# Optimization experiments

Measured on AMD Instinct MI355X. Metric: run time of the kernel, lower is better.

The kernel has to match this reference:

```python
import jax, jax.numpy as jnp
import numpy as np

B, N, L, K = 2, 16384, 256, 4
DIN, DOUT, DLAT, H, A, NH = 2, 3, 64, 128, 32, 4
PI = float(np.pi)

def _lin(key, din, dout, std=None):
    k1, k2 = jax.random.split(key)
    if std is None:
        lim = 1.0 / np.sqrt(din)
        w = jax.random.uniform(k1, (din, dout), minval=-lim, maxval=lim)
        b = jax.random.uniform(k2, (dout,), minval=-lim, maxval=lim)
        return w, b
    return jax.random.normal(k1, (din, dout)) * std

def setup_inputs() -> dict:
    key = jax.random.key(0)
    ks = jax.random.split(key, 16)
    x = jax.random.uniform(ks[0], (B, N, DIN)) * 2.0 - 1.0
    p = jax.random.uniform(ks[1], (B, L, DIN)) * 2.0 - 1.0
    c = jax.random.normal(ks[2], (B, L, DLAT))
    g = jax.random.uniform(ks[3], (B, L, 1)) * 0.5 + 0.1
    W_stem, b_stem = _lin(ks[4], DLAT, H)
    Wq_sin = _lin(ks[5], DIN, H // 2, std=2.0)
    Wq1, bq1 = _lin(ks[6], H + DIN, H)
    Wq2, bq2 = _lin(ks[7], H, NH * A)
    Wv_sin = _lin(ks[8], DIN, H // 2, std=20.0)
    Wv1, bv1 = _lin(ks[9], H + DIN, H)
    Wv2, bv2 = _lin(ks[10], H, 2 * H)
    Wk, bk = _lin(ks[11], H, NH * A)
    Wv, bv = _lin(ks[12], H, NH * H)
    Wo1, bo1 = _lin(ks[13], NH * H, NH * H)
    Wo2, bo2 = _lin(ks[14], NH * H, DOUT)
    return dict(x=x, p=p, c=c, g=g, W_stem=W_stem, b_stem=b_stem,
                Wq_sin=Wq_sin, Wq1=Wq1, bq1=bq1, Wq2=Wq2, bq2=bq2,
                Wv_sin=Wv_sin, Wv1=Wv1, bv1=bv1, Wv2=Wv2, bv2=bv2,
                Wk=Wk, bk=bk, Wv=Wv, bv=bv, Wo1=Wo1, bo1=bo1, Wo2=Wo2, bo2=bo2)

def _sin_emb(coords, W):
    c = PI * (coords + 1.0)
    e = c @ W
    return jnp.sin(jnp.concatenate([c, e, e + PI / 2.0], axis=-1))

def _emb_mlp(coords, Wsin, W1, b1, W2, b2):
    h = _sin_emb(coords, Wsin)
    h = jax.nn.gelu(h @ W1 + b1, approximate=False)
    return h @ W2 + b2

def _gather(t, idx):
    # t: [B,L,D], idx: [B,N,K] -> [B,N,K,D]
    return jax.vmap(lambda tb, ib: tb[ib])(t, idx)

def reference(x, p, c, g, W_stem, b_stem, Wq_sin, Wq1, bq1, Wq2, bq2,
              Wv_sin, Wv1, bv1, Wv2, bv2, Wk, bk, Wv, bv, Wo1, bo1, Wo2, bo2):
    c = c @ W_stem + b_stem                       # [B,L,H]
    k = c @ Wk + bk                               # [B,L,NH*A]
    rel_pos = x[:, :, None, :] - p[:, None, :, :] # [B,N,L,2]
    zx = jnp.sum(rel_pos ** 2, axis=-1)           # [B,N,L]
    idx = jnp.argsort(zx, axis=-1)[:, :, :K]      # [B,N,K]
    zx_k = jnp.take_along_axis(zx, idx, axis=2)[..., None]            # [B,N,K,1]
    rel_k = jnp.take_along_axis(rel_pos, idx[..., None], axis=2)      # [B,N,K,2]
    c_k = _gather(c, idx)                         # [B,N,K,H]
    k_k = _gather(k, idx)                         # [B,N,K,NH*A]
    g_k = _gather(g, idx)                         # [B,N,K,1]
    q = _emb_mlp(rel_k, Wq_sin, Wq1, bq1, Wq2, bq2)                   # [B,N,K,NH*A]
    vgb = _emb_mlp(rel_k, Wv_sin, Wv1, bv1, Wv2, bv2)                 # [B,N,K,2H]
    v_g, v_b = vgb[..., :H], vgb[..., H:]
    v = (c_k * v_g + v_b) @ Wv + bv               # [B,N,K,NH*H]
    q = q.reshape(B, N, K, NH, A)
    k_k = k_k.reshape(B, N, K, NH, A)
    v = v.reshape(B, N, K, NH, H)
    logits = jnp.sum(q * k_k, axis=-1, keepdims=True) \
             - ((1.0 / g_k ** 2) * zx_k)[..., None, :]                # [B,N,K,NH,1]
    att = jax.nn.softmax(logits, axis=2)
    y = jnp.sum(att * v, axis=2).reshape(B, N, NH * H)
    y = jax.nn.gelu(y @ Wo1 + bo1, approximate=False)
    return y @ Wo2 + bo2                          # [B,N,3]
```

## Files before the change

kernel.cpp:

```cpp
#include <hip/hip_runtime.h>
#include <math.h>

typedef unsigned short U16;
typedef unsigned int u32;
typedef unsigned long long u64;
typedef __attribute__((ext_vector_type(8))) short short8;
typedef __attribute__((ext_vector_type(4))) float f4;

#define LPTS   256
#define MFMA16(a,b,c) __builtin_amdgcn_mfma_f32_16x16x32_bf16(a, b, c, 0, 0, 0)

__device__ __forceinline__ float bf2f(U16 u) {
  return __uint_as_float(((unsigned int)u) << 16);
}
__device__ __forceinline__ U16 f2bf(float f) {
  unsigned int x = __float_as_uint(f);
  return (U16)((x + 0x7fffu + ((x >> 16) & 1u)) >> 16);
}
__device__ __forceinline__ float gelu_f(float v) {
  float z = fabsf(v) * 0.70710678f;
  float t = __builtin_amdgcn_rcpf(fmaf(0.3275911f, z, 1.0f));
  float poly = t * fmaf(t, fmaf(t, fmaf(t, fmaf(t, 1.061405429f, -1.453152027f),
                                        1.421413741f), -0.284496736f), 0.254829592f);
  float e = __expf(-z * z);
  float erf_abs = fmaf(-poly, e, 1.0f);
  float erf_s = copysignf(erf_abs, v);
  return 0.5f * v * (1.0f + erf_s);
}
__device__ __forceinline__ void ins4(u32& k0, u32& k1, u32& k2, u32& k3, u32 key) {
  if (key < k3) {
    if (key < k0)      { k3 = k2; k2 = k1; k1 = k0; k0 = key; }
    else if (key < k1) { k3 = k2; k2 = k1; k1 = key; }
    else if (key < k2) { k3 = k2; k2 = key; }
    else               { k3 = key; }
  }
}
__device__ __forceinline__ float ldf(const void* s, int i, int mode) {
  return mode ? bf2f(((const U16*)s)[i]) : ((const float*)s)[i];
}
__device__ __forceinline__ int wave_sniff(const void* w4) {
  int lane = threadIdx.x & 63;
  float v = bf2f(((const U16*)w4)[2 * lane]);
  u64 m = __ballot(fabsf(v) <= 0.1251f);
  return (__popcll(m) >= 56) ? 1 : 0;
}

struct PackArgs {
  const void* src[6];
  int K[6], N[6], KS[6];
  int base[7];
};

__global__ __launch_bounds__(256) void enf_prep(PackArgs pa,
    const void* c, const void* Wst, const void* bst, const void* Wkp, const void* bkp,
    float* __restrict__ cp_ws, float* __restrict__ kk_ws, U16* __restrict__ P)
{
  __shared__ float c_s[2][64];
  __shared__ float cp_s[2][128];
  const int t = threadIdx.x;
  const int mode = wave_sniff(Wst);
  const int bid = blockIdx.x;
  if (bid < 204) {
    int u = bid * 256 + t;
    if (u < pa.base[6]) {
      int s = 0;
      while (u >= pa.base[s + 1]) ++s;
      int rel = u - pa.base[s];
      int lane8 = rel & 63, rest = rel >> 6;
      int ks = rest % pa.KS[s], nt = rest / pa.KS[s];
      int kb = ks * 32 + ((lane8 >> 4) * 8);
      int n  = nt * 16 + (lane8 & 15);
      U16 vv[8];
#pragma unroll
      for (int j = 0; j < 8; ++j) {
        int k = kb + j;
        U16 v = 0;
        if (k < pa.K[s]) {
          int off = k * pa.N[s] + n;
          v = mode ? ((const U16*)pa.src[s])[off] : f2bf(((const float*)pa.src[s])[off]);
        }
        vv[j] = v;
      }
      *(short8*)(P + (size_t)u * 8) = *(short8*)vv;
    }
  } else {
    const int half = t >> 7, tl = t & 127;
    const int row = (bid - 204) * 2 + half;
    if (tl < 64) c_s[half][tl] = ldf(c, row * 64 + tl, mode);
    __syncthreads();
    float acc = 0.f;
#pragma unroll 8
    for (int i = 0; i < 64; ++i) acc = fmaf(c_s[half][i], ldf(Wst, i * 128 + tl, mode), acc);
    float cpv = acc + ldf(bst, tl, mode);
    cp_s[half][tl] = cpv;
    cp_ws[row * 128 + tl] = cpv;
    __syncthreads();
    acc = 0.f;
#pragma unroll 8
    for (int i = 0; i < 128; ++i) acc = fmaf(cp_s[half][i], ldf(Wkp, i * 128 + tl, mode), acc);
    kk_ws[row * 128 + tl] = acc + ldf(bkp, tl, mode);
  }
}

__global__ __launch_bounds__(512, 8) void enf_main(
    const void* __restrict__ w4,
    const void* __restrict__ x, const void* __restrict__ p, const void* __restrict__ g,
    const void* __restrict__ Wq_sin, const void* __restrict__ Wv_sin,
    const U16* __restrict__ PWq1, const void* __restrict__ bq1,
    const U16* __restrict__ PWq2, const void* __restrict__ bq2,
    const U16* __restrict__ PWv1, const void* __restrict__ bv1,
    const U16* __restrict__ PWv2, const void* __restrict__ bv2,
    const U16* __restrict__ PWv, const void* __restrict__ bv,
    const U16* __restrict__ PWo1, const void* __restrict__ bo1,
    const void* __restrict__ Wo2, const void* __restrict__ bo2,
    const float* __restrict__ cp_ws, const float* __restrict__ kk_ws,
    void* __restrict__ outp)
{
  __shared__ __align__(16) U16 poolS[64 * 168];
  __shared__ __align__(16) U16 poolH[64 * 132];
  __shared__ float wsin_s[128];
  __shared__ float xq[32];
  __shared__ float selDx[64], selDy[64], selB[64];
  __shared__ float att_s[64 * 4];
  __shared__ U16   selL[64];

  const int t = threadIdx.x;
  const int w = t >> 6, lane = t & 63;
  const int quad = lane >> 4, cl = lane & 15;
  const int qbase = blockIdx.x * 16;
  const int b = qbase >> 14;
  const int mode = wave_sniff(w4);
  float* p_sh = (float*)poolS;

  if (t < 32) xq[t] = ldf(x, qbase * 2 + t, mode);
  if (t < 128) wsin_s[t] = ldf(Wq_sin, t, mode);
  p_sh[t] = ldf(p, b * LPTS * 2 + t, mode);
  __syncthreads();

  {
    const int q = t >> 5;
    const float x0 = xq[q * 2 + 0], x1 = xq[q * 2 + 1];
    const int j = t & 31;
    u32 k0 = ~0u, k1 = ~0u, k2 = ~0u, k3 = ~0u;
#pragma unroll
    for (int s = 0; s < 8; ++s) {
      const int l = j * 8 + s;
      float dx = __fsub_rn(x0, p_sh[l * 2 + 0]);
      float dy = __fsub_rn(x1, p_sh[l * 2 + 1]);
      float d  = __fadd_rn(__fmul_rn(dx, dx), __fmul_rn(dy, dy));
      u32 key = (__float_as_uint(d) & 0xFFFFFF00u) | (u32)l;
      ins4(k0, k1, k2, k3, key);
    }
#pragma unroll
    for (int d = 1; d <= 16; d <<= 1) {
      u32 p0 = __shfl_xor(k0, d, 32);
      u32 p1 = __shfl_xor(k1, d, 32);
      u32 p2 = __shfl_xor(k2, d, 32);
      u32 p3 = __shfl_xor(k3, d, 32);
      ins4(k0, k1, k2, k3, p0); ins4(k0, k1, k2, k3, p1);
      ins4(k0, k1, k2, k3, p2); ins4(k0, k1, k2, k3, p3);
    }
    if (j == 0) {
      u32 sel[4] = { k0, k1, k2, k3 };
#pragma unroll
      for (int k = 0; k < 4; ++k) {
        int l = (int)(sel[k] & 255u);
        int r = q * 4 + k;
        selL[r]  = (U16)l;
        float dx = __fsub_rn(x0, p_sh[l * 2 + 0]);
        float dy = __fsub_rn(x1, p_sh[l * 2 + 1]);
        float zx = __fadd_rn(__fmul_rn(dx, dx), __fmul_rn(dy, dy));
        selDx[r] = dx;
        selDy[r] = dy;
        float gf = ldf(g, b * LPTS + l, mode);
        selB[r]  = __fmul_rn(1.0f / __fmul_rn(gf, gf), zx);
      }
    }
  }
  __syncthreads();

  {
    const int r = t >> 3, ln = t & 7;
    const float dx = selDx[r], dy = selDy[r];
    const float c0 = 3.14159274f * (dx + 1.0f);
    const float c1 = 3.14159274f * (dy + 1.0f);
    if (ln == 0) poolS[r * 168 + 0] = f2bf(__sinf(c0));
    if (ln == 1) poolS[r * 168 + 1] = f2bf(__sinf(c1));
#pragma unroll 1
    for (int i = ln; i < 64; i += 8) {
      float e = __fadd_rn(__fmul_rn(c0, wsin_s[i]), __fmul_rn(c1, wsin_s[64 + i]));
      poolS[r * 168 + 2 + i]  = f2bf(__sinf(e));
      poolS[r * 168 + 66 + i] = f2bf(__sinf(e + 1.57079637f));
    }
#pragma unroll 1
    for (int i = 130 + ln; i < 160; i += 8) poolS[r * 168 + i] = 0;
  }
  __syncthreads();

  if (t < 128) wsin_s[t] = ldf(Wv_sin, t, mode);
  {
    f4 acc[4] = {{0,0,0,0},{0,0,0,0},{0,0,0,0},{0,0,0,0}};
    const U16* pb0 = PWq1 + ((w * 5) * 64 + lane) * 8;
    short8 b0 = *(const short8*)(pb0);
#pragma unroll 1
    for (int ks = 0; ks < 5; ++ks) {
      short8 n0 = *(const short8*)(pb0 + (ks + 1) * 512);
#pragma unroll
      for (int mt = 0; mt < 4; ++mt) {
        short8 a = *(const short8*)(poolS + (mt * 16 + cl) * 168 + quad * 8 + ks * 32);
        acc[mt] = MFMA16(a, b0, acc[mt]);
      }
      b0 = n0;
    }
    int col = w * 16 + cl;
    float bb = ldf(bq1, col, mode);
#pragma unroll
    for (int mt = 0; mt < 4; ++mt)
#pragma unroll
      for (int reg = 0; reg < 4; ++reg)
        poolH[(mt * 16 + quad * 4 + reg) * 132 + col] = f2bf(gelu_f(acc[mt][reg] + bb));
  }
  __syncthreads();

  if (w < 4) {
    const int wl = w;
    f4 acc[2][4] = {{{0,0,0,0},{0,0,0,0},{0,0,0,0},{0,0,0,0}},
                    {{0,0,0,0},{0,0,0,0},{0,0,0,0},{0,0,0,0}}};
    const U16* pb0 = PWq2 + ((2 * wl + 0) * 4 * 64 + lane) * 8;
    const U16* pb1 = PWq2 + ((2 * wl + 1) * 4 * 64 + lane) * 8;
    short8 b0 = *(const short8*)(pb0);
    short8 b1 = *(const short8*)(pb1);
#pragma unroll 1
    for (int ks = 0; ks < 4; ++ks) {
      short8 n0 = *(const short8*)(pb0 + (ks + 1) * 512);
      short8 n1 = *(const short8*)(pb1 + (ks + 1) * 512);
#pragma unroll
      for (int mt = 0; mt < 4; ++mt) {
        short8 a = *(const short8*)(poolH + (mt * 16 + cl) * 132 + quad * 8 + ks * 32);
        acc[0][mt] = MFMA16(a, b0, acc[0][mt]);
        acc[1][mt] = MFMA16(a, b1, acc[1][mt]);
      }
      b0 = n0; b1 = n1;
    }
    const float bq2c0 = ldf(bq2, (2 * wl + 0) * 16 + cl, mode);
    const float bq2c1 = ldf(bq2, (2 * wl + 1) * 16 + cl, mode);
    const float* kkb = kk_ws + (size_t)b * LPTS * 128;
#pragma unroll
    for (int mt = 0; mt < 4; ++mt) {
      float part[4];
#pragma unroll
      for (int reg = 0; reg < 4; ++reg) {
        int r = mt * 16 + quad * 4 + reg;
        const float* kr = kkb + selL[r] * 128;
        float q0 = acc[0][mt][reg] + bq2c0;
        float q1 = acc[1][mt][reg] + bq2c1;
        part[reg] = __fmul_rn(q0, kr[(2 * wl + 0) * 16 + cl]);
        part[reg] = fmaf(q1, kr[(2 * wl + 1) * 16 + cl], part[reg]);
      }
#pragma unroll
      for (int d = 1; d <= 8; d <<= 1) {
        part[0] += __shfl_xor(part[0], d, 16);
        part[1] += __shfl_xor(part[1], d, 16);
        part[2] += __shfl_xor(part[2], d, 16);
        part[3] += __shfl_xor(part[3], d, 16);
      }
      if (cl == 0) {
        int q = mt * 4 + quad;
        float lg[4];
#pragma unroll
        for (int reg = 0; reg < 4; ++reg)
          lg[reg] = part[reg] - selB[q * 4 + reg];
        float m = fmaxf(fmaxf(lg[0], lg[1]), fmaxf(lg[2], lg[3]));
        float e0 = __expf(lg[0] - m), e1 = __expf(lg[1] - m);
        float e2 = __expf(lg[2] - m), e3 = __expf(lg[3] - m);
        float s = ((e0 + e1) + e2) + e3;
        att_s[(q * 4 + 0) * 4 + wl] = e0 / s;
        att_s[(q * 4 + 1) * 4 + wl] = e1 / s;
        att_s[(q * 4 + 2) * 4 + wl] = e2 / s;
        att_s[(q * 4 + 3) * 4 + wl] = e3 / s;
      }
    }
  } else {
    const int tt = t - 256;
    const int r = tt >> 2, ln = tt & 3;
    const float dx = selDx[r], dy = selDy[r];
    const float c0 = 3.14159274f * (dx + 1.0f);
    const float c1 = 3.14159274f * (dy + 1.0f);
    if (ln == 0) poolS[r * 168 + 0] = f2bf(__sinf(c0));
    if (ln == 1) poolS[r * 168 + 1] = f2bf(__sinf(c1));
#pragma unroll 1
    for (int i = ln; i < 64; i += 4) {
      float e = __fadd_rn(__fmul_rn(c0, wsin_s[i]), __fmul_rn(c1, wsin_s[64 + i]));
      poolS[r * 168 + 2 + i]  = f2bf(__sinf(e));
      poolS[r * 168 + 66 + i] = f2bf(__sinf(e + 1.57079637f));
    }
#pragma unroll 1
    for (int i = 130 + ln; i < 160; i += 4) poolS[r * 168 + i] = 0;
  }
  __syncthreads();

  {
    f4 acc[4] = {{0,0,0,0},{0,0,0,0},{0,0,0,0},{0,0,0,0}};
    const U16* pb0 = PWv1 + ((w * 5) * 64 + lane) * 8;
    short8 b0 = *(const short8*)(pb0);
#pragma unroll 1
    for (int ks = 0; ks < 5; ++ks) {
      short8 n0 = *(const short8*)(pb0 + (ks + 1) * 512);
#pragma unroll
      for (int mt = 0; mt < 4; ++mt) {
        short8 a = *(const short8*)(poolS + (mt * 16 + cl) * 168 + quad * 8 + ks * 32);
        acc[mt] = MFMA16(a, b0, acc[mt]);
      }
      b0 = n0;
    }
    int col = w * 16 + cl;
    float bb = ldf(bv1, col, mode);
#pragma unroll
    for (int mt = 0; mt < 4; ++mt)
#pragma unroll
      for (int reg = 0; reg < 4; ++reg)
        poolH[(mt * 16 + quad * 4 + reg) * 132 + col] = f2bf(gelu_f(acc[mt][reg] + bb));
  }
  __syncthreads();

  {
    f4 ag[4] = {{0,0,0,0},{0,0,0,0},{0,0,0,0},{0,0,0,0}};
    f4 ab[4] = {{0,0,0,0},{0,0,0,0},{0,0,0,0},{0,0,0,0}};
    const U16* pg = PWv2 + ((w * 4) * 64 + lane) * 8;
    const U16* pb = PWv2 + (((8 + w) * 4) * 64 + lane) * 8;
    short8 bg = *(const short8*)(pg);
    short8 bb2 = *(const short8*)(pb);
#pragma unroll 1
    for (int ks = 0; ks < 4; ++ks) {
      short8 ng = *(const short8*)(pg + (ks + 1) * 512);
      short8 nb = *(const short8*)(pb + (ks + 1) * 512);
#pragma unroll
      for (int mt = 0; mt < 4; ++mt) {
        short8 a = *(const short8*)(poolH + (mt * 16 + cl) * 132 + quad * 8 + ks * 32);
        ag[mt] = MFMA16(a, bg, ag[mt]);
        ab[mt] = MFMA16(a, bb2, ab[mt]);
      }
      bg = ng; bb2 = nb;
    }
    int col = w * 16 + cl;
    float bgb = ldf(bv2, col, mode), bbb = ldf(bv2, 128 + col, mode);
#pragma unroll
    for (int mt = 0; mt < 4; ++mt)
#pragma unroll
      for (int reg = 0; reg < 4; ++reg) {
        int row = mt * 16 + quad * 4 + reg;
        float cp = cp_ws[(b * LPTS + selL[row]) * 128 + col];
        float vin = __fadd_rn(__fmul_rn(cp, ag[mt][reg] + bgb), ab[mt][reg] + bbb);
        poolS[row * 132 + col] = f2bf(vin);
      }
  }
  __syncthreads();

  {
    const int gqh = t >> 3, sl = t & 7;
    const int q = gqh & 15, h = gqh >> 4;
    float a0 = att_s[(q * 4 + 0) * 4 + h];
    float a1 = att_s[(q * 4 + 1) * 4 + h];
    float a2 = att_s[(q * 4 + 2) * 4 + h];
    float a3 = att_s[(q * 4 + 3) * 4 + h];
#pragma unroll 1
    for (int j = 0; j < 4; ++j) {
      int e0 = j * 32 + sl * 4;
      ushort4 v0 = *(const ushort4*)(poolS + (q * 4 + 0) * 132 + e0);
      ushort4 v1 = *(const ushort4*)(poolS + (q * 4 + 1) * 132 + e0);
      ushort4 v2 = *(const ushort4*)(poolS + (q * 4 + 2) * 132 + e0);
      ushort4 v3 = *(const ushort4*)(poolS + (q * 4 + 3) * 132 + e0);
      ushort4 o;
      o.x = f2bf(fmaf(a3, bf2f(v3.x), fmaf(a2, bf2f(v2.x), fmaf(a1, bf2f(v1.x), a0 * bf2f(v0.x)))));
      o.y = f2bf(fmaf(a3, bf2f(v3.y), fmaf(a2, bf2f(v2.y), fmaf(a1, bf2f(v1.y), a0 * bf2f(v0.y)))));
      o.z = f2bf(fmaf(a3, bf2f(v3.z), fmaf(a2, bf2f(v2.z), fmaf(a1, bf2f(v1.z), a0 * bf2f(v0.z)))));
      o.w = f2bf(fmaf(a3, bf2f(v3.w), fmaf(a2, bf2f(v2.w), fmaf(a1, bf2f(v1.w), a0 * bf2f(v0.w)))));
      *(ushort4*)(poolH + (h * 16 + q) * 132 + e0) = o;
    }
  }
  __syncthreads();

  U16* ySt = poolS;
  {
    f4 acc5[4] = {{0,0,0,0},{0,0,0,0},{0,0,0,0},{0,0,0,0}};
    const int h = w >> 1;
    const int nt0 = h * 8 + (w & 1) * 4;
    const U16* a5p = poolH + (h * 16 + cl) * 132 + quad * 8;
    short8 cb[4], nb[4];
#pragma unroll
    for (int ntl = 0; ntl < 4; ++ntl)
      cb[ntl] = *(const short8*)(PWv + ((nt0 + ntl) * 4 * 64 + lane) * 8);
#pragma unroll 1
    for (int ks = 0; ks < 4; ++ks) {
#pragma unroll
      for (int ntl = 0; ntl < 4; ++ntl)
        nb[ntl] = *(const short8*)(PWv + (((nt0 + ntl) * 4 + ks + 1) * 64 + lane) * 8);
      short8 a = *(const short8*)(a5p + ks * 32);
#pragma unroll
      for (int ntl = 0; ntl < 4; ++ntl) acc5[ntl] = MFMA16(a, cb[ntl], acc5[ntl]);
#pragma unroll
      for (int ntl = 0; ntl < 4; ++ntl) cb[ntl] = nb[ntl];
    }
#pragma unroll
    for (int ntl = 0; ntl < 4; ++ntl) {
      int col = (nt0 + ntl) * 16 + cl;
      float bbv = ldf(bv, col, mode);
#pragma unroll
      for (int reg = 0; reg < 4; ++reg) {
        int q = quad * 4 + reg;
        ySt[q * 520 + col] = f2bf(acc5[ntl][reg] + bbv);
      }
    }
  }
  __syncthreads();

  {
    f4 acc[4] = {{0,0,0,0},{0,0,0,0},{0,0,0,0},{0,0,0,0}};
    const U16* aP = ySt + cl * 520 + quad * 8;
    const U16* bP = PWo1 + ((w * 4) * 16 * 64 + lane) * 8;
    short8 cb[4], nb[4];
#pragma unroll
    for (int ntl = 0; ntl < 4; ++ntl)
      cb[ntl] = *(const short8*)(bP + (ntl * 16) * 512);
#pragma unroll 1
    for (int ks = 0; ks < 16; ++ks) {
#pragma unroll
      for (int ntl = 0; ntl < 4; ++ntl)
        nb[ntl] = *(const short8*)(bP + (ntl * 16 + ks + 1) * 512);
      short8 a = *(const short8*)(aP + ks * 32);
#pragma unroll
      for (int ntl = 0; ntl < 4; ++ntl) acc[ntl] = MFMA16(a, cb[ntl], acc[ntl]);
#pragma unroll
      for (int ntl = 0; ntl < 4; ++ntl) cb[ntl] = nb[ntl];
    }
    float oacc[4][3];
#pragma unroll
    for (int reg = 0; reg < 4; ++reg) { oacc[reg][0]=0.f; oacc[reg][1]=0.f; oacc[reg][2]=0.f; }
#pragma unroll
    for (int ntl = 0; ntl < 4; ++ntl) {
      int col = (w * 4 + ntl) * 16 + cl;
      float bb = ldf(bo1, col, mode);
      float w0 = ldf(Wo2, col * 3 + 0, mode);
      float w1 = ldf(Wo2, col * 3 + 1, mode);
      float w2 = ldf(Wo2, col * 3 + 2, mode);
#pragma unroll
      for (int reg = 0; reg < 4; ++reg) {
        float y2 = gelu_f(acc[ntl][reg] + bb);
        oacc[reg][0] = fmaf(y2, w0, oacc[reg][0]);
        oacc[reg][1] = fmaf(y2, w1, oacc[reg][1]);
        oacc[reg][2] = fmaf(y2, w2, oacc[reg][2]);
      }
    }
    float* obuf = (float*)poolH;
#pragma unroll
    for (int reg = 0; reg < 4; ++reg)
#pragma unroll
      for (int cix = 0; cix < 3; ++cix) {
        float v = oacc[reg][cix];
        v += __shfl_xor(v, 1);
        v += __shfl_xor(v, 2);
        v += __shfl_xor(v, 4);
        v += __shfl_xor(v, 8);
        if (cl == 0) obuf[(w * 16 + quad * 4 + reg) * 3 + cix] = v;
      }
  }
  __syncthreads();
  if (t < 48) {
    float* obuf = (float*)poolH;
    int row = t / 3, cix = t - row * 3;
    float s = obuf[row * 3 + cix];
#pragma unroll
    for (int ww = 1; ww < 8; ++ww) s += obuf[(ww * 16 + row) * 3 + cix];
    float ov = s + ldf(bo2, cix, mode);
    int pos = (qbase + row) * 3 + cix;
    if (mode) ((U16*)outp)[pos] = f2bf(ov);
    else      ((float*)outp)[pos] = ov;
  }
}

extern "C" void kernel_launch(void* const* d_in, const int* in_sizes, int n_in,
                              void* d_out, int out_size, void* d_ws, size_t ws_size,
                              hipStream_t stream) {
  (void)in_sizes; (void)n_in; (void)out_size; (void)ws_size;

  float* ws     = (float*)d_ws;
  float* cp_ws  = ws;
  float* kk_ws  = ws + 65536;
  U16*   Pbase  = (U16*)(ws + 131072);
  U16*   PWq1   = Pbase + 0;
  U16*   PWq2   = Pbase + 20480;
  U16*   PWv1   = Pbase + 36864;
  U16*   PWv2   = Pbase + 57344;
  U16*   PWv    = Pbase + 90112;
  U16*   PWo1   = Pbase + 155648;

  PackArgs pa;
  const int psrc[6] = {7, 9, 12, 14, 18, 20};
  static const int pK[6]  = {130, 128, 130, 128, 128, 512};
  static const int pN[6]  = {128, 128, 128, 256, 512, 512};
  static const int pKS[6] = {5, 4, 5, 4, 4, 16};
  static const int pB8[7] = {0, 2560, 4608, 7168, 11264, 19456, 52224};
  for (int i = 0; i < 6; ++i) {
    pa.src[i] = d_in[psrc[i]];
    pa.K[i] = pK[i]; pa.N[i] = pN[i]; pa.KS[i] = pKS[i]; pa.base[i] = pB8[i];
  }
  pa.base[6] = pB8[6];

  hipLaunchKernelGGL(enf_prep, dim3(460), dim3(256), 0, stream,
                     pa, d_in[2], d_in[4], d_in[5], d_in[16], d_in[17],
                     cp_ws, kk_ws, Pbase);
  hipLaunchKernelGGL(enf_main, dim3(2048), dim3(512), 0, stream,
                     d_in[4],
                     d_in[0], d_in[1], d_in[3],
                     d_in[6], d_in[11],
                     PWq1, d_in[8],  PWq2, d_in[10],
                     PWv1, d_in[13], PWv2, d_in[15],
                     PWv,  d_in[19],
                     PWo1, d_in[21], d_in[22], d_in[23],
                     cp_ws, kk_ws, (void*)d_out);
}
```

Before: 281.3 us.

## Process 32 queries per block to double MFMA reuse of weight fragments

Doubles the number of query points per workgroup from 16 to 32 (128 neighbor rows), halving the grid and giving each wave twice as many M-tiles per loaded weight fragment across all the MLP and projection GEMMs. The goal is to halve the global/L2 traffic for the packed weights per query and amortise per-block setup such as the p load and the kNN staging. In exchange, LDS use and accumulator registers roughly double, and launch bounds drop to 4 blocks per SM, which lowers occupancy and latency hiding.

```diff
diff --git a/kernel.cpp b/kernel.cpp
--- a/kernel.cpp
+++ b/kernel.cpp
@@ -102,7 +102,7 @@
   }
 }
 
-__global__ __launch_bounds__(512, 8) void enf_main(
+__global__ __launch_bounds__(512, 4) void enf_main(
     const void* __restrict__ w4,
     const void* __restrict__ x, const void* __restrict__ p, const void* __restrict__ g,
     const void* __restrict__ Wq_sin, const void* __restrict__ Wv_sin,
@@ -116,35 +116,34 @@
     const float* __restrict__ cp_ws, const float* __restrict__ kk_ws,
     void* __restrict__ outp)
 {
-  __shared__ __align__(16) U16 poolS[64 * 168];
-  __shared__ __align__(16) U16 poolH[64 * 132];
+  __shared__ __align__(16) U16 poolS[128 * 168];
+  __shared__ __align__(16) U16 poolH[128 * 132];
   __shared__ float wsin_s[128];
-  __shared__ float xq[32];
-  __shared__ float selDx[64], selDy[64], selB[64];
-  __shared__ float att_s[64 * 4];
-  __shared__ U16   selL[64];
-
+  __shared__ float xq[64];
+  __shared__ float selDx[128], selDy[128], selB[128];
+  __shared__ float att_s[128 * 4];
+  __shared__ U16   selL[128];
   const int t = threadIdx.x;
   const int w = t >> 6, lane = t & 63;
   const int quad = lane >> 4, cl = lane & 15;
-  const int qbase = blockIdx.x * 16;
+  const int qbase = blockIdx.x * 32;
   const int b = qbase >> 14;
   const int mode = wave_sniff(w4);
   float* p_sh = (float*)poolS;
 
-  if (t < 32) xq[t] = ldf(x, qbase * 2 + t, mode);
+  if (t < 64) xq[t] = ldf(x, qbase * 2 + t, mode);
   if (t < 128) wsin_s[t] = ldf(Wq_sin, t, mode);
   p_sh[t] = ldf(p, b * LPTS * 2 + t, mode);
   __syncthreads();
 
   {
-    const int q = t >> 5;
+    const int q = t >> 4;
     const float x0 = xq[q * 2 + 0], x1 = xq[q * 2 + 1];
-    const int j = t & 31;
+    const int j = t & 15;
     u32 k0 = ~0u, k1 = ~0u, k2 = ~0u, k3 = ~0u;
 #pragma unroll
-    for (int s = 0; s < 8; ++s) {
-      const int l = j * 8 + s;
+    for (int s = 0; s < 16; ++s) {
+      const int l = j * 16 + s;
       float dx = __fsub_rn(x0, p_sh[l * 2 + 0]);
       float dy = __fsub_rn(x1, p_sh[l * 2 + 1]);
       float d  = __fadd_rn(__fmul_rn(dx, dx), __fmul_rn(dy, dy));
@@ -152,11 +151,11 @@
       ins4(k0, k1, k2, k3, key);
     }
 #pragma unroll
-    for (int d = 1; d <= 16; d <<= 1) {
-      u32 p0 = __shfl_xor(k0, d, 32);
-      u32 p1 = __shfl_xor(k1, d, 32);
-      u32 p2 = __shfl_xor(k2, d, 32);
-      u32 p3 = __shfl_xor(k3, d, 32);
+    for (int d = 1; d <= 8; d <<= 1) {
+      u32 p0 = __shfl_xor(k0, d, 16);
+      u32 p1 = __shfl_xor(k1, d, 16);
+      u32 p2 = __shfl_xor(k2, d, 16);
+      u32 p3 = __shfl_xor(k3, d, 16);
       ins4(k0, k1, k2, k3, p0); ins4(k0, k1, k2, k3, p1);
       ins4(k0, k1, k2, k3, p2); ins4(k0, k1, k2, k3, p3);
     }
@@ -180,33 +179,35 @@
   __syncthreads();
 
   {
-    const int r = t >> 3, ln = t & 7;
+    const int r = t >> 2, ln = t & 3;
     const float dx = selDx[r], dy = selDy[r];
     const float c0 = 3.14159274f * (dx + 1.0f);
     const float c1 = 3.14159274f * (dy + 1.0f);
     if (ln == 0) poolS[r * 168 + 0] = f2bf(__sinf(c0));
     if (ln == 1) poolS[r * 168 + 1] = f2bf(__sinf(c1));
 #pragma unroll 1
-    for (int i = ln; i < 64; i += 8) {
+    for (int i = ln; i < 64; i += 4) {
       float e = __fadd_rn(__fmul_rn(c0, wsin_s[i]), __fmul_rn(c1, wsin_s[64 + i]));
       poolS[r * 168 + 2 + i]  = f2bf(__sinf(e));
       poolS[r * 168 + 66 + i] = f2bf(__sinf(e + 1.57079637f));
     }
 #pragma unroll 1
-    for (int i = 130 + ln; i < 160; i += 8) poolS[r * 168 + i] = 0;
+    for (int i = 130 + ln; i < 160; i += 4) poolS[r * 168 + i] = 0;
   }
   __syncthreads();
 
   if (t < 128) wsin_s[t] = ldf(Wv_sin, t, mode);
   {
-    f4 acc[4] = {{0,0,0,0},{0,0,0,0},{0,0,0,0},{0,0,0,0}};
+    f4 acc[8];
+#pragma unroll
+    for (int i = 0; i < 8; ++i) acc[i] = (f4){0.f, 0.f, 0.f, 0.f};
     const U16* pb0 = PWq1 + ((w * 5) * 64 + lane) * 8;
     short8 b0 = *(const short8*)(pb0);
 #pragma unroll 1
     for (int ks = 0; ks < 5; ++ks) {
       short8 n0 = *(const short8*)(pb0 + (ks + 1) * 512);
 #pragma unroll
-      for (int mt = 0; mt < 4; ++mt) {
+      for (int mt = 0; mt < 8; ++mt) {
         short8 a = *(const short8*)(poolS + (mt * 16 + cl) * 168 + quad * 8 + ks * 32);
         acc[mt] = MFMA16(a, b0, acc[mt]);
       }
@@ -215,7 +216,7 @@
     int col = w * 16 + cl;
     float bb = ldf(bq1, col, mode);
 #pragma unroll
-    for (int mt = 0; mt < 4; ++mt)
+    for (int mt = 0; mt < 8; ++mt)
 #pragma unroll
       for (int reg = 0; reg < 4; ++reg)
         poolH[(mt * 16 + quad * 4 + reg) * 132 + col] = f2bf(gelu_f(acc[mt][reg] + bb));
@@ -224,8 +225,9 @@
 
   if (w < 4) {
     const int wl = w;
-    f4 acc[2][4] = {{{0,0,0,0},{0,0,0,0},{0,0,0,0},{0,0,0,0}},
-                    {{0,0,0,0},{0,0,0,0},{0,0,0,0},{0,0,0,0}}};
+    f4 acc[2][8];
+#pragma unroll
+    for (int i = 0; i < 8; ++i) { acc[0][i] = (f4){0.f,0.f,0.f,0.f}; acc[1][i] = (f4){0.f,0.f,0.f,0.f}; }
     const U16* pb0 = PWq2 + ((2 * wl + 0) * 4 * 64 + lane) * 8;
     const U16* pb1 = PWq2 + ((2 * wl + 1) * 4 * 64 + lane) * 8;
     short8 b0 = *(const short8*)(pb0);
@@ -235,7 +237,7 @@
       short8 n0 = *(const short8*)(pb0 + (ks + 1) * 512);
       short8 n1 = *(const short8*)(pb1 + (ks + 1) * 512);
 #pragma unroll
-      for (int mt = 0; mt < 4; ++mt) {
+      for (int mt = 0; mt < 8; ++mt) {
         short8 a = *(const short8*)(poolH + (mt * 16 + cl) * 132 + quad * 8 + ks * 32);
         acc[0][mt] = MFMA16(a, b0, acc[0][mt]);
         acc[1][mt] = MFMA16(a, b1, acc[1][mt]);
@@ -246,7 +248,7 @@
     const float bq2c1 = ldf(bq2, (2 * wl + 1) * 16 + cl, mode);
     const float* kkb = kk_ws + (size_t)b * LPTS * 128;
 #pragma unroll
-    for (int mt = 0; mt < 4; ++mt) {
+    for (int mt = 0; mt < 8; ++mt) {
       float part[4];
 #pragma unroll
       for (int reg = 0; reg < 4; ++reg) {
@@ -282,32 +284,34 @@
     }
   } else {
     const int tt = t - 256;
-    const int r = tt >> 2, ln = tt & 3;
+    const int r = tt >> 1, ln = tt & 1;
     const float dx = selDx[r], dy = selDy[r];
     const float c0 = 3.14159274f * (dx + 1.0f);
     const float c1 = 3.14159274f * (dy + 1.0f);
     if (ln == 0) poolS[r * 168 + 0] = f2bf(__sinf(c0));
     if (ln == 1) poolS[r * 168 + 1] = f2bf(__sinf(c1));
 #pragma unroll 1
-    for (int i = ln; i < 64; i += 4) {
+    for (int i = ln; i < 64; i += 2) {
       float e = __fadd_rn(__fmul_rn(c0, wsin_s[i]), __fmul_rn(c1, wsin_s[64 + i]));
       poolS[r * 168 + 2 + i]  = f2bf(__sinf(e));
       poolS[r * 168 + 66 + i] = f2bf(__sinf(e + 1.57079637f));
     }
 #pragma unroll 1
-    for (int i = 130 + ln; i < 160; i += 4) poolS[r * 168 + i] = 0;
-  }
-  __syncthreads();
-
-  {
-    f4 acc[4] = {{0,0,0,0},{0,0,0,0},{0,0,0,0},{0,0,0,0}};
+    for (int i = 130 + ln; i < 160; i += 2) poolS[r * 168 + i] = 0;
+  }
+  __syncthreads();
+
+  {
+    f4 acc[8];
+#pragma unroll
+    for (int i = 0; i < 8; ++i) acc[i] = (f4){0.f, 0.f, 0.f, 0.f};
     const U16* pb0 = PWv1 + ((w * 5) * 64 + lane) * 8;
     short8 b0 = *(const short8*)(pb0);
 #pragma unroll 1
     for (int ks = 0; ks < 5; ++ks) {
       short8 n0 = *(const short8*)(pb0 + (ks + 1) * 512);
 #pragma unroll
-      for (int mt = 0; mt < 4; ++mt) {
+      for (int mt = 0; mt < 8; ++mt) {
         short8 a = *(const short8*)(poolS + (mt * 16 + cl) * 168 + quad * 8 + ks * 32);
         acc[mt] = MFMA16(a, b0, acc[mt]);
       }
@@ -316,7 +320,7 @@
     int col = w * 16 + cl;
     float bb = ldf(bv1, col, mode);
 #pragma unroll
-    for (int mt = 0; mt < 4; ++mt)
+    for (int mt = 0; mt < 8; ++mt)
 #pragma unroll
       for (int reg = 0; reg < 4; ++reg)
         poolH[(mt * 16 + quad * 4 + reg) * 132 + col] = f2bf(gelu_f(acc[mt][reg] + bb));
@@ -324,8 +328,9 @@
   __syncthreads();
 
   {
-    f4 ag[4] = {{0,0,0,0},{0,0,0,0},{0,0,0,0},{0,0,0,0}};
-    f4 ab[4] = {{0,0,0,0},{0,0,0,0},{0,0,0,0},{0,0,0,0}};
+    f4 ag[8], ab[8];
+#pragma unroll
+    for (int i = 0; i < 8; ++i) { ag[i] = (f4){0.f,0.f,0.f,0.f}; ab[i] = (f4){0.f,0.f,0.f,0.f}; }
     const U16* pg = PWv2 + ((w * 4) * 64 + lane) * 8;
     const U16* pb = PWv2 + (((8 + w) * 4) * 64 + lane) * 8;
     short8 bg = *(const short8*)(pg);
@@ -335,7 +340,7 @@
       short8 ng = *(const short8*)(pg + (ks + 1) * 512);
       short8 nb = *(const short8*)(pb + (ks + 1) * 512);
 #pragma unroll
-      for (int mt = 0; mt < 4; ++mt) {
+      for (int mt = 0; mt < 8; ++mt) {
         short8 a = *(const short8*)(poolH + (mt * 16 + cl) * 132 + quad * 8 + ks * 32);
         ag[mt] = MFMA16(a, bg, ag[mt]);
         ab[mt] = MFMA16(a, bb2, ab[mt]);
@@ -345,7 +350,7 @@
     int col = w * 16 + cl;
     float bgb = ldf(bv2, col, mode), bbb = ldf(bv2, 128 + col, mode);
 #pragma unroll
-    for (int mt = 0; mt < 4; ++mt)
+    for (int mt = 0; mt < 8; ++mt)
 #pragma unroll
       for (int reg = 0; reg < 4; ++reg) {
         int row = mt * 16 + quad * 4 + reg;
@@ -357,15 +362,15 @@
   __syncthreads();
 
   {
-    const int gqh = t >> 3, sl = t & 7;
-    const int q = gqh & 15, h = gqh >> 4;
+    const int gqh = t >> 2, sl = t & 3;
+    const int q = gqh & 31, h = gqh >> 5;
     float a0 = att_s[(q * 4 + 0) * 4 + h];
     float a1 = att_s[(q * 4 + 1) * 4 + h];
     float a2 = att_s[(q * 4 + 2) * 4 + h];
     float a3 = att_s[(q * 4 + 3) * 4 + h];
 #pragma unroll 1
-    for (int j = 0; j < 4; ++j) {
-      int e0 = j * 32 + sl * 4;
+    for (int j = 0; j < 8; ++j) {
+      int e0 = j * 16 + sl * 4;
       ushort4 v0 = *(const ushort4*)(poolS + (q * 4 + 0) * 132 + e0);
       ushort4 v1 = *(const ushort4*)(poolS + (q * 4 + 1) * 132 + e0);
       ushort4 v2 = *(const ushort4*)(poolS + (q * 4 + 2) * 132 + e0);
@@ -375,17 +380,19 @@
       o.y = f2bf(fmaf(a3, bf2f(v3.y), fmaf(a2, bf2f(v2.y), fmaf(a1, bf2f(v1.y), a0 * bf2f(v0.y)))));
       o.z = f2bf(fmaf(a3, bf2f(v3.z), fmaf(a2, bf2f(v2.z), fmaf(a1, bf2f(v1.z), a0 * bf2f(v0.z)))));
       o.w = f2bf(fmaf(a3, bf2f(v3.w), fmaf(a2, bf2f(v2.w), fmaf(a1, bf2f(v1.w), a0 * bf2f(v0.w)))));
-      *(ushort4*)(poolH + (h * 16 + q) * 132 + e0) = o;
+      *(ushort4*)(poolH + (h * 32 + q) * 132 + e0) = o;
     }
   }
   __syncthreads();
 
   U16* ySt = poolS;
   {
-    f4 acc5[4] = {{0,0,0,0},{0,0,0,0},{0,0,0,0},{0,0,0,0}};
+    f4 acc5[2][4];
+#pragma unroll
+    for (int i = 0; i < 4; ++i) { acc5[0][i] = (f4){0.f,0.f,0.f,0.f}; acc5[1][i] = (f4){0.f,0.f,0.f,0.f}; }
     const int h = w >> 1;
     const int nt0 = h * 8 + (w & 1) * 4;
-    const U16* a5p = poolH + (h * 16 + cl) * 132 + quad * 8;
+    const U16* a5p = poolH + (h * 32 + cl) * 132 + quad * 8;
     short8 cb[4], nb[4];
 #pragma unroll
     for (int ntl = 0; ntl < 4; ++ntl)
@@ -395,9 +402,12 @@
 #pragma unroll
       for (int ntl = 0; ntl < 4; ++ntl)
         nb[ntl] = *(const short8*)(PWv + (((nt0 + ntl) * 4 + ks + 1) * 64 + lane) * 8);
-      short8 a = *(const short8*)(a5p + ks * 32);
-#pragma unroll
-      for (int ntl = 0; ntl < 4; ++ntl) acc5[ntl] = MFMA16(a, cb[ntl], acc5[ntl]);
+#pragma unroll
+      for (int mt = 0; mt < 2; ++mt) {
+        short8 a = *(const short8*)(a5p + mt * 16 * 132 + ks * 32);
+#pragma unroll
+        for (int ntl = 0; ntl < 4; ++ntl) acc5[mt][ntl] = MFMA16(a, cb[ntl], acc5[mt][ntl]);
+      }
 #pragma unroll
       for (int ntl = 0; ntl < 4; ++ntl) cb[ntl] = nb[ntl];
     }
@@ -406,16 +416,20 @@
       int col = (nt0 + ntl) * 16 + cl;
       float bbv = ldf(bv, col, mode);
 #pragma unroll
-      for (int reg = 0; reg < 4; ++reg) {
-        int q = quad * 4 + reg;
-        ySt[q * 520 + col] = f2bf(acc5[ntl][reg] + bbv);
-      }
-    }
-  }
-  __syncthreads();
-
-  {
-    f4 acc[4] = {{0,0,0,0},{0,0,0,0},{0,0,0,0},{0,0,0,0}};
+      for (int mt = 0; mt < 2; ++mt)
+#pragma unroll
+        for (int reg = 0; reg < 4; ++reg) {
+          int q = mt * 16 + quad * 4 + reg;
+          ySt[q * 520 + col] = f2bf(acc5[mt][ntl][reg] + bbv);
+        }
+    }
+  }
+  __syncthreads();
+
+  {
+    f4 acc[2][4];
+#pragma unroll
+    for (int i = 0; i < 4; ++i) { acc[0][i] = (f4){0.f,0.f,0.f,0.f}; acc[1][i] = (f4){0.f,0.f,0.f,0.f}; }
     const U16* aP = ySt + cl * 520 + quad * 8;
     const U16* bP = PWo1 + ((w * 4) * 16 * 64 + lane) * 8;
     short8 cb[4], nb[4];
@@ -427,15 +441,20 @@
 #pragma unroll
       for (int ntl = 0; ntl < 4; ++ntl)
         nb[ntl] = *(const short8*)(bP + (ntl * 16 + ks + 1) * 512);
-      short8 a = *(const short8*)(aP + ks * 32);
-#pragma unroll
-      for (int ntl = 0; ntl < 4; ++ntl) acc[ntl] = MFMA16(a, cb[ntl], acc[ntl]);
+#pragma unroll
+      for (int mt = 0; mt < 2; ++mt) {
+        short8 a = *(const short8*)(aP + mt * 16 * 520 + ks * 32);
+#pragma unroll
+        for (int ntl = 0; ntl < 4; ++ntl) acc[mt][ntl] = MFMA16(a, cb[ntl], acc[mt][ntl]);
+      }
 #pragma unroll
       for (int ntl = 0; ntl < 4; ++ntl) cb[ntl] = nb[ntl];
     }
-    float oacc[4][3];
-#pragma unroll
-    for (int reg = 0; reg < 4; ++reg) { oacc[reg][0]=0.f; oacc[reg][1]=0.f; oacc[reg][2]=0.f; }
+    float oacc[2][4][3];
+#pragma unroll
+    for (int mt = 0; mt < 2; ++mt)
+#pragma unroll
+      for (int reg = 0; reg < 4; ++reg) { oacc[mt][reg][0]=0.f; oacc[mt][reg][1]=0.f; oacc[mt][reg][2]=0.f; }
 #pragma unroll
     for (int ntl = 0; ntl < 4; ++ntl) {
       int col = (w * 4 + ntl) * 16 + cl;
@@ -444,33 +463,37 @@
       float w1 = ldf(Wo2, col * 3 + 1, mode);
       float w2 = ldf(Wo2, col * 3 + 2, mode);
 #pragma unroll
-      for (int reg = 0; reg < 4; ++reg) {
-        float y2 = gelu_f(acc[ntl][reg] + bb);
-        oacc[reg][0] = fmaf(y2, w0, oacc[reg][0]);
-        oacc[reg][1] = fmaf(y2, w1, oacc[reg][1]);
-        oacc[reg][2] = fmaf(y2, w2, oacc[reg][2]);
-      }
+      for (int mt = 0; mt < 2; ++mt)
+#pragma unroll
+        for (int reg = 0; reg < 4; ++reg) {
+          float y2 = gelu_f(acc[mt][ntl][reg] + bb);
+          oacc[mt][reg][0] = fmaf(y2, w0, oacc[mt][reg][0]);
+          oacc[mt][reg][1] = fmaf(y2, w1, oacc[mt][reg][1]);
+          oacc[mt][reg][2] = fmaf(y2, w2, oacc[mt][reg][2]);
+        }
     }
     float* obuf = (float*)poolH;
 #pragma unroll
-    for (int reg = 0; reg < 4; ++reg)
-#pragma unroll
-      for (int cix = 0; cix < 3; ++cix) {
-        float v = oacc[reg][cix];
-        v += __shfl_xor(v, 1);
-        v += __shfl_xor(v, 2);
-        v += __shfl_xor(v, 4);
-        v += __shfl_xor(v, 8);
-        if (cl == 0) obuf[(w * 16 + quad * 4 + reg) * 3 + cix] = v;
-      }
-  }
-  __syncthreads();
-  if (t < 48) {
+    for (int mt = 0; mt < 2; ++mt)
+#pragma unroll
+      for (int reg = 0; reg < 4; ++reg)
+#pragma unroll
+        for (int cix = 0; cix < 3; ++cix) {
+          float v = oacc[mt][reg][cix];
+          v += __shfl_xor(v, 1);
+          v += __shfl_xor(v, 2);
+          v += __shfl_xor(v, 4);
+          v += __shfl_xor(v, 8);
+          if (cl == 0) obuf[(w * 32 + mt * 16 + quad * 4 + reg) * 3 + cix] = v;
+        }
+  }
+  __syncthreads();
+  if (t < 96) {
     float* obuf = (float*)poolH;
     int row = t / 3, cix = t - row * 3;
     float s = obuf[row * 3 + cix];
 #pragma unroll
-    for (int ww = 1; ww < 8; ++ww) s += obuf[(ww * 16 + row) * 3 + cix];
+    for (int ww = 1; ww < 8; ++ww) s += obuf[(ww * 32 + row) * 3 + cix];
     float ov = s + ldf(bo2, cix, mode);
     int pos = (qbase + row) * 3 + cix;
     if (mode) ((U16*)outp)[pos] = f2bf(ov);
@@ -509,7 +532,7 @@
   hipLaunchKernelGGL(enf_prep, dim3(460), dim3(256), 0, stream,
                      pa, d_in[2], d_in[4], d_in[5], d_in[16], d_in[17],
                      cp_ws, kk_ws, Pbase);
-  hipLaunchKernelGGL(enf_main, dim3(2048), dim3(512), 0, stream,
+  hipLaunchKernelGGL(enf_main, dim3(1024), dim3(512), 0, stream,
                      d_in[4],
                      d_in[0], d_in[1], d_in[3],
                      d_in[6], d_in[11],
```

Measured after the change: 268.4 us. -4.6%, faster.
